# Performance work log

Hardware: AMD Instinct MI355X
Metric: run time of the kernel (lower is better)

## Reference

```python
import jax, jax.numpy as jnp
import numpy as np

D_IN = 512
SEQ_LEN = 4096
CHUNK = 256
NUM_CHUNKS = SEQ_LEN // CHUNK
BATCH = 4


def _xavier_uniform(key, d_in, d_out):
    limit = float(np.sqrt(6.0 / (d_in + d_out)))
    return jax.random.uniform(key, (d_in, d_out), dtype=jnp.float32, minval=-limit, maxval=limit)


def _logit(p, eps=1e-06):
    p = min(max(p, eps), 1.0 - eps)
    return jnp.asarray(np.log(p / (1.0 - p)), dtype=jnp.float32)


def setup_inputs() -> dict:
    key = jax.random.key(0)
    ks = jax.random.split(key, 6)
    x = jax.random.normal(ks[0], (BATCH, SEQ_LEN, D_IN), dtype=jnp.float32)
    return {
        "x": x,
        "w_q": _xavier_uniform(ks[1], D_IN, D_IN),
        "w_k": _xavier_uniform(ks[2], D_IN, D_IN),
        "w_v": _xavier_uniform(ks[3], D_IN, D_IN),
        "mem_w1": _xavier_uniform(ks[4], D_IN, 2 * D_IN),
        "mem_w2": _xavier_uniform(ks[5], 2 * D_IN, D_IN),
        "alpha_t": _logit(0.001),  # unconstrained; sigmoid -> alpha
        "lr_t": _logit(0.01),
        "decay_t": _logit(0.9),
        "update_mem": 1,
    }


def _mem_fwd(h, W1, W2):
    # LinearMLPMemory depth=2: x @ W1 -> gelu -> @ W2 (torch F.gelu is exact erf)
    return jax.nn.gelu(h @ W1, approximate=False) @ W2


def reference(x, w_q, w_k, w_v, mem_w1, mem_w2, alpha_t, lr_t, decay_t, update_mem):
    alpha = jax.nn.sigmoid(alpha_t)
    lr = jax.nn.sigmoid(lr_t)
    decay = jax.nn.sigmoid(decay_t)

    def loss_fn(Ws, k, v):
        W1, W2 = Ws
        pred = _mem_fwd(k, W1, W2)
        return jnp.mean((pred - v) ** 2)

    grad_fn = jax.grad(loss_fn)

    def step(carry, chunk):
        # chunk: [B, CHUNK, D]
        W1, W2, S1, S2 = carry
        k = chunk @ w_k
        v = chunk @ w_v
        g1, g2 = grad_fn((W1, W2), k, v)
        S1 = decay * S1 - lr * g1  # surprise (momentum of negative grads)
        S2 = decay * S2 - lr * g2
        W1 = (1.0 - alpha) * W1 + S1  # weight decay + surprise update
        W2 = (1.0 - alpha) * W2 + S2
        return (W1, W2, S1, S2), None

    W1, W2 = mem_w1, mem_w2
    if update_mem:
        B, S, D = x.shape
        # [NUM_CHUNKS, B, CHUNK, D]: sequential store over chunks (parallelize=False)
        chunks = x.reshape(B, NUM_CHUNKS, CHUNK, D).transpose(1, 0, 2, 3)
        init = (W1, W2, jnp.zeros_like(W1), jnp.zeros_like(W2))
        (W1, W2, _, _), _ = jax.lax.scan(step, init, chunks)

    q = x @ w_q
    return _mem_fwd(q, W1, W2)
```

## Files before the change

kernel.cpp:

```cpp
#include <hip/hip_runtime.h>
#include <math.h>

#define D_IN    512
#define HID     1024
#define CHUNK_L 256
#define NCHUNK  16
#define SEQ_L   4096
#define ROWS    1024
#define NROWS_T 16384

typedef __attribute__((ext_vector_type(4))) float f32x4;
typedef __attribute__((ext_vector_type(8))) short bf16x8;
typedef __attribute__((ext_vector_type(4))) short bf16x4;

#define LOSS_SCALE (2.0f / 524288.0f)

__device__ __forceinline__ float gelu_f(float v) {
    return v * 0.5f * (1.0f + erff(v * 0.70710678118654752f));
}
__device__ __forceinline__ float dgelu_f(float v) {
    float cdf = 0.5f * (1.0f + erff(v * 0.70710678118654752f));
    float pdf = 0.3989422804014327f * expf(-0.5f * v * v);
    return cdf + v * pdf;
}
__device__ __forceinline__ float sigmoid_dev(float x) { return 1.0f / (1.0f + expf(-x)); }
__device__ __forceinline__ short f2b(float f) {
    unsigned u = __float_as_uint(f);
    u += 0x7fffu + ((u >> 16) & 1u);
    return (short)(u >> 16);
}
__device__ __forceinline__ float b2f(short s) {
    return __uint_as_float(((unsigned)(unsigned short)s) << 16);
}
__device__ __forceinline__ float read_scalar(const float* p) {
    float v = *p;
    if (fabsf(v) > 0.5f && fabsf(v) < 16.0f) return v;
    unsigned short lo = ((const unsigned short*)p)[0];
    return __uint_as_float(((unsigned)lo) << 16);
}

__device__ __forceinline__ void glds16(const short* g, short* l) {
    __builtin_amdgcn_global_load_lds(
        (const __attribute__((address_space(1))) void*)g,
        (__attribute__((address_space(3))) void*)l, 16, 0, 0);
}

template<int NKB>
__device__ __forceinline__ void tile_gemm2(
    const short* __restrict__ A, int lda,
    const short* __restrict__ B, int ldb,
    int m0, int n0, short* KB, f32x4 acc[2][2])
{
    const int tid = threadIdx.x;
    const int lane = tid & 63, wave = tid >> 6;
    const int wy = (wave >> 1) * 32, wx = (wave & 1) * 32;
    const int l16 = lane & 15, q = lane >> 4;

    const int ga = tid, gb = tid + 256;
    const int ra = ga >> 3, ja = ga & 7;
    const int rb = gb >> 3, jb = gb & 7;
    const short* sA0 = A + (size_t)(m0 + ra) * lda + ((ja ^ (ra & 7)) << 3);
    const short* sA1 = A + (size_t)(m0 + rb) * lda + ((jb ^ (rb & 7)) << 3);
    const short* sB0 = B + (size_t)(n0 + ra) * ldb + ((ja ^ (ra & 7)) << 3);
    const short* sB1 = B + (size_t)(n0 + rb) * ldb + ((jb ^ (rb & 7)) << 3);

    f32x4 z = {0.f, 0.f, 0.f, 0.f};
    acc[0][0] = z; acc[0][1] = z; acc[1][0] = z; acc[1][1] = z;

    auto issue = [&](int kb) {
        const int ko = kb << 6;
        short* d = KB + (kb & 3) * 8192 + wave * 512;
        glds16(sA0 + ko, d);
        glds16(sA1 + ko, d + 2048);
        glds16(sB0 + ko, d + 4096);
        glds16(sB1 + ko, d + 6144);
    };
    issue(0); issue(1); issue(2);

#pragma unroll
    for (int j = 0; j < NKB; ++j) {
        if (NKB - 1 - j >= 2)      asm volatile("s_waitcnt vmcnt(8)" ::: "memory");
        else if (NKB - 1 - j == 1) asm volatile("s_waitcnt vmcnt(4)" ::: "memory");
        else                       asm volatile("s_waitcnt vmcnt(0)" ::: "memory");
        __builtin_amdgcn_s_barrier();
        __builtin_amdgcn_sched_barrier(0);
        if (j + 3 < NKB) issue(j + 3);
        const short* sl = KB + (j & 3) * 8192;
#pragma unroll
        for (int ks = 0; ks < 2; ++ks) {
            bf16x8 af[2], bf[2];
#pragma unroll
            for (int i = 0; i < 2; ++i) {
                int row = wy + i * 16 + l16;
                af[i] = *(const bf16x8*)&sl[(row << 6) + (((ks * 4 + q) ^ (row & 7)) << 3)];
            }
#pragma unroll
            for (int jj = 0; jj < 2; ++jj) {
                int row = wx + jj * 16 + l16;
                bf[jj] = *(const bf16x8*)&sl[4096 + (row << 6) + (((ks * 4 + q) ^ (row & 7)) << 3)];
            }
#pragma unroll
            for (int i = 0; i < 2; ++i)
#pragma unroll
                for (int jj = 0; jj < 2; ++jj)
                    acc[i][jj] = __builtin_amdgcn_mfma_f32_16x16x32_bf16(af[i], bf[jj], acc[i][jj], 0, 0, 0);
        }
    }
}

template<bool CHUNKA>
__device__ __forceinline__ void tile_gemm_f32(
    const float* __restrict__ Af, int lda, int t,
    const short* __restrict__ B, int ldb, int K,
    int m0, int n0, short* As, short* Bs, f32x4 acc[2][2])
{
    const int tid = threadIdx.x;
    const int lane = tid & 63, wave = tid >> 6;
    const int wy = (wave >> 1) * 32, wx = (wave & 1) * 32;
    const int l16 = lane & 15, q = lane >> 4;
    const int r0 = tid >> 3, r1 = r0 + 32, c8 = (tid & 7) * 8;

    auto arow = [&](int r) -> size_t {
        if (CHUNKA) return (size_t)(r >> 8) * SEQ_L + (size_t)t * CHUNK_L + (r & 255);
        return (size_t)r;
    };
    const size_t ga0 = arow(m0 + r0) * (size_t)lda + c8;
    const size_t ga1 = arow(m0 + r1) * (size_t)lda + c8;
    const size_t gb0 = (size_t)(n0 + r0) * ldb + c8;
    const size_t gb1 = (size_t)(n0 + r1) * ldb + c8;

    f32x4 fa0[2], fa1[2];
    bf16x8 rb0, rb1;

    auto load_tiles = [&](int k0) {
        fa0[0] = *(const f32x4*)&Af[ga0 + k0];
        fa0[1] = *(const f32x4*)&Af[ga0 + k0 + 4];
        fa1[0] = *(const f32x4*)&Af[ga1 + k0];
        fa1[1] = *(const f32x4*)&Af[ga1 + k0 + 4];
        rb0 = *(const bf16x8*)&B[gb0 + k0];
        rb1 = *(const bf16x8*)&B[gb1 + k0];
    };
    auto store_tiles = [&]() {
        bf16x8 p0, p1;
#pragma unroll
        for (int u = 0; u < 4; ++u) {
            p0[u] = f2b(fa0[0][u]); p0[u + 4] = f2b(fa0[1][u]);
            p1[u] = f2b(fa1[0][u]); p1[u + 4] = f2b(fa1[1][u]);
        }
        *(bf16x8*)&As[r0 * 72 + c8] = p0;
        *(bf16x8*)&As[r1 * 72 + c8] = p1;
        *(bf16x8*)&Bs[r0 * 72 + c8] = rb0;
        *(bf16x8*)&Bs[r1 * 72 + c8] = rb1;
    };

    f32x4 z = {0.f, 0.f, 0.f, 0.f};
    acc[0][0] = z; acc[0][1] = z; acc[1][0] = z; acc[1][1] = z;

    const int nkb = K >> 6;
    load_tiles(0);
    for (int kb = 0; kb < nkb; ++kb) {
        store_tiles();
        __syncthreads();
        if (kb + 1 < nkb) load_tiles((kb + 1) << 6);
#pragma unroll
        for (int ks = 0; ks < 2; ++ks) {
            bf16x8 af[2], bf[2];
#pragma unroll
            for (int i = 0; i < 2; ++i)
                af[i] = *(const bf16x8*)&As[(wy + i * 16 + l16) * 72 + ks * 32 + q * 8];
#pragma unroll
            for (int j = 0; j < 2; ++j)
                bf[j] = *(const bf16x8*)&Bs[(wx + j * 16 + l16) * 72 + ks * 32 + q * 8];
#pragma unroll
            for (int i = 0; i < 2; ++i)
#pragma unroll
                for (int j = 0; j < 2; ++j)
                    acc[i][j] = __builtin_amdgcn_mfma_f32_16x16x32_bf16(af[i], bf[j], acc[i][j], 0, 0, 0);
        }
        __syncthreads();
    }
}

#define EPI_IDX() \
    const int tid_ = threadIdx.x; \
    const int wy_  = ((tid_ >> 6) >> 1) * 32; \
    const int wxl_ = ((tid_ >> 6) & 1) * 32; \
    const int q4_  = ((tid_ & 63) >> 4) * 4; \
    const int l16_ = tid_ & 15;

__global__ __launch_bounds__(256)
void init_all(const float* __restrict__ w_q, const float* __restrict__ w_k,
              const float* __restrict__ w_v, const float* __restrict__ m1,
              const float* __restrict__ m2,
              float* __restrict__ W1f, float* __restrict__ W2f,
              float* __restrict__ S1, float* __restrict__ S2,
              short* __restrict__ WkvT, short* __restrict__ wqT,
              short* __restrict__ W1bT, short* __restrict__ W2bT,
              short* __restrict__ W2b0, short* __restrict__ W2b1)
{
    int i = blockIdx.x * 256 + threadIdx.x;
    float w1 = m1[i], w2 = m2[i];
    W1f[i] = w1; S1[i] = 0.f;
    W2f[i] = w2; S2[i] = 0.f;
    short w2b = f2b(w2);
    W2b0[i] = w2b; W2b1[i] = w2b;
    int n9 = i >> 9, k9 = i & 511;
    W1bT[i] = f2b(m1[(size_t)k9 * HID + n9]);
    WkvT[i] = f2b(n9 < 512 ? w_k[(size_t)k9 * D_IN + n9]
                           : w_v[(size_t)k9 * D_IN + (n9 - 512)]);
    if (i < 262144) wqT[i] = f2b(w_q[(size_t)k9 * D_IN + n9]);
    int n10 = i >> 10, k10 = i & 1023;
    W2bT[i] = f2b(m2[(size_t)k10 * D_IN + n10]);
}

__global__ __launch_bounds__(256)
void kvq_kernel(const float* __restrict__ x, const short* __restrict__ WkvT,
                const short* __restrict__ wqT,
                short* __restrict__ KVall, short* __restrict__ Ktall,
                short* __restrict__ qall)
{
    __shared__ short As[64 * 72];
    __shared__ short Bs[64 * 72];
    const int bid = blockIdx.x;
    EPI_IDX();
    f32x4 acc[2][2];
    if (bid < 4096) {
        int t = bid >> 8, tile = bid & 255;
        int m0 = (tile >> 4) * 64, n0 = (tile & 15) * 64;
        tile_gemm_f32<true>(x, D_IN, t, WkvT, D_IN, D_IN, m0, n0, As, Bs, acc);
        short* KV = KVall + (size_t)t * ROWS * 1024;
        short* Kt = Ktall + (size_t)t * D_IN * 1024;
#pragma unroll
        for (int i = 0; i < 2; ++i)
#pragma unroll
            for (int j = 0; j < 2; ++j) {
                int m = m0 + wy_ + i * 16 + q4_, n = n0 + wxl_ + j * 16 + l16_;
                bf16x4 pk;
#pragma unroll
                for (int r = 0; r < 4; ++r) {
                    short b = f2b(acc[i][j][r]);
                    KV[(size_t)(m + r) * 1024 + n] = b;
                    pk[r] = b;
                }
                if (n < 512) *(bf16x4*)&Kt[(size_t)n * 1024 + m] = pk;
            }
    } else {
        int idx = bid - 4096;
        int m0 = (idx >> 3) * 64, n0 = (idx & 7) * 64;
        tile_gemm_f32<false>(x, D_IN, 0, wqT, D_IN, D_IN, m0, n0, As, Bs, acc);
#pragma unroll
        for (int i = 0; i < 2; ++i)
#pragma unroll
            for (int j = 0; j < 2; ++j) {
                int m = m0 + wy_ + i * 16 + q4_, n = n0 + wxl_ + j * 16 + l16_;
#pragma unroll
                for (int r = 0; r < 4; ++r)
                    qall[(size_t)(m + r) * D_IN + n] = f2b(acc[i][j][r]);
            }
    }
}

__global__ __launch_bounds__(256)
void h_kernel(const short* __restrict__ KVt, const short* __restrict__ W1bT,
              short* __restrict__ Gb, short* __restrict__ GbT, short* __restrict__ DG)
{
    __shared__ short KB[4 * 2 * 4096];
    const int bid = blockIdx.x;
    EPI_IDX();
    int m0 = (bid >> 4) * 64, n0 = (bid & 15) * 64;
    f32x4 acc[2][2];
    tile_gemm2<8>(KVt, 1024, W1bT, D_IN, m0, n0, KB, acc);
#pragma unroll
    for (int i = 0; i < 2; ++i)
#pragma unroll
        for (int j = 0; j < 2; ++j) {
            int m = m0 + wy_ + i * 16 + q4_, n = n0 + wxl_ + j * 16 + l16_;
            bf16x4 pg;
#pragma unroll
            for (int r = 0; r < 4; ++r) {
                float v = acc[i][j][r];
                float g = gelu_f(v);
                Gb[(size_t)(m + r) * 1024 + n] = f2b(g);
                DG[(size_t)(m + r) * 1024 + n] = f2b(dgelu_f(v));
                pg[r] = f2b(g);
            }
            *(bf16x4*)&GbT[(size_t)n * 1024 + m] = pg;
        }
}

__global__ __launch_bounds__(256)
void e_kernel(const short* __restrict__ Gb, const short* __restrict__ W2bT,
              short* __restrict__ KVt, short* __restrict__ EVt)
{
    __shared__ short KB[4 * 2 * 4096];
    const int bid = blockIdx.x;
    EPI_IDX();
    int m0 = (bid >> 3) * 64, n0 = (bid & 7) * 64;
    f32x4 acc[2][2];
    tile_gemm2<16>(Gb, HID, W2bT, HID, m0, n0, KB, acc);
#pragma unroll
    for (int i = 0; i < 2; ++i)
#pragma unroll
        for (int j = 0; j < 2; ++j) {
            int m = m0 + wy_ + i * 16 + q4_, n = n0 + wxl_ + j * 16 + l16_;
            bf16x4 pe;
#pragma unroll
            for (int r = 0; r < 4; ++r) {
                size_t ci = (size_t)(m + r) * 1024 + 512 + n;
                float e = (acc[i][j][r] - b2f(KVt[ci])) * LOSS_SCALE;
                KVt[ci] = f2b(e);
                pe[r] = f2b(e);
            }
            *(bf16x4*)&EVt[(size_t)n * 1024 + m] = pe;
        }
}

__global__ __launch_bounds__(256)
void dhg2_kernel(const short* __restrict__ KVt, const short* __restrict__ W2bP,
                 const short* __restrict__ DG, short* __restrict__ DHt,
                 const short* __restrict__ GbT, const short* __restrict__ EVt,
                 float* __restrict__ W2f, float* __restrict__ S2,
                 short* __restrict__ W2bT, short* __restrict__ W2bN,
                 const float* __restrict__ ap, const float* __restrict__ lp,
                 const float* __restrict__ dp, const int* __restrict__ um)
{
    __shared__ short KB[4 * 2 * 4096];
    const int bid = blockIdx.x;
    EPI_IDX();
    f32x4 acc[2][2];
    if (bid < 256) {
        int m0 = (bid >> 4) * 64, n0 = (bid & 15) * 64;
        tile_gemm2<8>(KVt + 512, 1024, W2bP, D_IN, m0, n0, KB, acc);
#pragma unroll
        for (int i = 0; i < 2; ++i)
#pragma unroll
            for (int j = 0; j < 2; ++j) {
                int m = m0 + wy_ + i * 16 + q4_, n = n0 + wxl_ + j * 16 + l16_;
                bf16x4 pd;
#pragma unroll
                for (int r = 0; r < 4; ++r)
                    pd[r] = f2b(acc[i][j][r] * b2f(DG[(size_t)(m + r) * 1024 + n]));
                *(bf16x4*)&DHt[(size_t)n * 1024 + m] = pd;
            }
    } else {
        int idx = bid - 256;
        int m0 = (idx >> 3) * 64, n0 = (idx & 7) * 64;
        tile_gemm2<16>(GbT, ROWS, EVt, ROWS, m0, n0, KB, acc);
        if (*um != 0) {
            const float alpha = sigmoid_dev(read_scalar(ap));
            const float lr    = sigmoid_dev(read_scalar(lp));
            const float decay = sigmoid_dev(read_scalar(dp));
#pragma unroll
            for (int i = 0; i < 2; ++i)
#pragma unroll
                for (int j = 0; j < 2; ++j) {
                    int m = m0 + wy_ + i * 16 + q4_, n = n0 + wxl_ + j * 16 + l16_;
                    bf16x4 pw;
#pragma unroll
                    for (int r = 0; r < 4; ++r) {
                        size_t ci = (size_t)(m + r) * D_IN + n;
                        float s = decay * S2[ci] - lr * acc[i][j][r];
                        S2[ci] = s;
                        float w = (1.0f - alpha) * W2f[ci] + s;
                        W2f[ci] = w;
                        W2bN[ci] = f2b(w);
                        pw[r] = f2b(w);
                    }
                    *(bf16x4*)&W2bT[(size_t)n * 1024 + m] = pw;
                }
        }
    }
}

__global__ __launch_bounds__(256)
void g1_kernel(const short* __restrict__ Ktt, const short* __restrict__ DHt,
               float* __restrict__ W1f, float* __restrict__ S1,
               short* __restrict__ W1bT,
               const float* __restrict__ ap, const float* __restrict__ lp,
               const float* __restrict__ dp, const int* __restrict__ um)
{
    __shared__ short KB[4 * 2 * 4096];
    const int bid = blockIdx.x;
    EPI_IDX();
    int m0 = (bid >> 4) * 64, n0 = (bid & 15) * 64;
    f32x4 acc[2][2];
    tile_gemm2<16>(Ktt, ROWS, DHt, ROWS, m0, n0, KB, acc);
    if (*um != 0) {
        const float alpha = sigmoid_dev(read_scalar(ap));
        const float lr    = sigmoid_dev(read_scalar(lp));
        const float decay = sigmoid_dev(read_scalar(dp));
#pragma unroll
        for (int i = 0; i < 2; ++i)
#pragma unroll
            for (int j = 0; j < 2; ++j) {
                int m = m0 + wy_ + i * 16 + q4_, n = n0 + wxl_ + j * 16 + l16_;
                bf16x4 pw;
#pragma unroll
                for (int r = 0; r < 4; ++r) {
                    size_t ci = (size_t)(m + r) * HID + n;
                    float s = decay * S1[ci] - lr * acc[i][j][r];
                    S1[ci] = s;
                    float w = (1.0f - alpha) * W1f[ci] + s;
                    W1f[ci] = w;
                    pw[r] = f2b(w);
                }
                *(bf16x4*)&W1bT[(size_t)n * D_IN + m] = pw;
            }
    }
}

__global__ __launch_bounds__(256)
void ro_h_kernel(const short* __restrict__ qall, const short* __restrict__ W1bT,
                 short* __restrict__ Hro)
{
    __shared__ short KB[4 * 2 * 4096];
    const int bid = blockIdx.x;
    EPI_IDX();
    int m0 = (bid >> 4) * 64, n0 = (bid & 15) * 64;
    f32x4 acc[2][2];
    tile_gemm2<8>(qall, D_IN, W1bT, D_IN, m0, n0, KB, acc);
#pragma unroll
    for (int i = 0; i < 2; ++i)
#pragma unroll
        for (int j = 0; j < 2; ++j) {
            int m = m0 + wy_ + i * 16 + q4_, n = n0 + wxl_ + j * 16 + l16_;
#pragma unroll
            for (int r = 0; r < 4; ++r)
                Hro[(size_t)(m + r) * HID + n] = f2b(gelu_f(acc[i][j][r]));
        }
}

__global__ __launch_bounds__(256)
void ro_o_kernel(const short* __restrict__ Hro, const short* __restrict__ W2bT,
                 float* __restrict__ out)
{
    __shared__ short KB[4 * 2 * 4096];
    const int bid = blockIdx.x;
    EPI_IDX();
    int m0 = (bid >> 3) * 64, n0 = (bid & 7) * 64;
    f32x4 acc[2][2];
    tile_gemm2<16>(Hro, HID, W2bT, HID, m0, n0, KB, acc);
#pragma unroll
    for (int i = 0; i < 2; ++i)
#pragma unroll
        for (int j = 0; j < 2; ++j) {
            int m = m0 + wy_ + i * 16 + q4_, n = n0 + wxl_ + j * 16 + l16_;
#pragma unroll
            for (int r = 0; r < 4; ++r)
                out[(size_t)(m + r) * D_IN + n] = acc[i][j][r];
        }
}

extern "C" void kernel_launch(void* const* d_in, const int* in_sizes, int n_in,
                              void* d_out, int out_size, void* d_ws, size_t ws_size,
                              hipStream_t stream)
{
    const float* x      = (const float*)d_in[0];
    const float* w_q    = (const float*)d_in[1];
    const float* w_k    = (const float*)d_in[2];
    const float* w_v    = (const float*)d_in[3];
    const float* mem_w1 = (const float*)d_in[4];
    const float* mem_w2 = (const float*)d_in[5];
    const float* ap     = (const float*)d_in[6];
    const float* lp     = (const float*)d_in[7];
    const float* dpp    = (const float*)d_in[8];
    const int*   um     = (const int*)d_in[9];
    float* out = (float*)d_out;

    const int nW = D_IN * HID;
    float* W1f = (float*)d_ws;
    float* W2f = W1f + nW;
    float* S1  = W2f + nW;
    float* S2  = S1 + nW;
    short* p   = (short*)(S2 + nW);
    short* WkvT = p;            p += nW;
    short* wqT  = p;            p += 256 * 1024;
    short* W1bT = p;            p += nW;
    short* W2bT = p;            p += nW;
    short* W2b0 = p;            p += nW;
    short* W2b1 = p;            p += nW;
    short* Gb   = p;            p += ROWS * HID;
    short* GbT  = p;            p += ROWS * HID;
    short* DG   = p;            p += ROWS * HID;
    short* EVt  = p;            p += ROWS * D_IN;
    short* DHt  = p;            p += ROWS * HID;
    short* qall = p;            p += (size_t)NROWS_T * D_IN;
    short* KVall = p;           p += (size_t)NCHUNK * ROWS * 1024;
    short* Ktall = p;           p += (size_t)NCHUNK * D_IN * 1024;
    short* Hro  = p;            p += (size_t)NROWS_T * HID;

    dim3 blk(256);
    hipLaunchKernelGGL(init_all, dim3(nW / 256), blk, 0, stream,
                       w_q, w_k, w_v, mem_w1, mem_w2,
                       W1f, W2f, S1, S2, WkvT, wqT, W1bT, W2bT, W2b0, W2b1);
    hipLaunchKernelGGL(kvq_kernel, dim3(6144), blk, 0, stream,
                       x, WkvT, wqT, KVall, Ktall, qall);

    for (int t = 0; t < NCHUNK; ++t) {
        short* KVt  = KVall + (size_t)t * ROWS * 1024;
        short* Ktt  = Ktall + (size_t)t * D_IN * 1024;
        short* W2bP = (t & 1) ? W2b1 : W2b0;
        short* W2bN = (t & 1) ? W2b0 : W2b1;
        hipLaunchKernelGGL(h_kernel, dim3(256), blk, 0, stream, KVt, W1bT, Gb, GbT, DG);
        hipLaunchKernelGGL(e_kernel, dim3(128), blk, 0, stream, Gb, W2bT, KVt, EVt);
        hipLaunchKernelGGL(dhg2_kernel, dim3(384), blk, 0, stream,
                           KVt, W2bP, DG, DHt, GbT, EVt, W2f, S2, W2bT, W2bN,
                           ap, lp, dpp, um);
        hipLaunchKernelGGL(g1_kernel, dim3(128), blk, 0, stream,
                           Ktt, DHt, W1f, S1, W1bT, ap, lp, dpp, um);
    }

    hipLaunchKernelGGL(ro_h_kernel, dim3(4096), blk, 0, stream, qall, W1bT, Hro);
    hipLaunchKernelGGL(ro_o_kernel, dim3(2048), blk, 0, stream, Hro, W2bT, out);
}
```

Measured before the change: 826.3 us.

## Pre-convert x to bf16 and use shared GEMM path with M-fastest tile order

Adds a kernel that converts x to bf16 once, so the projection GEMM can use the same pipelined bf16 tile routine as the other GEMMs instead of a float-loading variant that converts on every tile load. The separate f32 tile routine is removed. All kernels also remap block index to tile so consecutive blocks walk along M and share the same B (weight) tile, which should improve L2 reuse of weights. The cost is an extra kernel launch and a bf16 copy of x in the workspace.

Measured after the change: 801.3 us. 3.0% less time.

```diff
diff --git a/kernel.cpp b/kernel.cpp
--- a/kernel.cpp
+++ b/kernel.cpp
@@ -105,79 +105,6 @@
                 for (int jj = 0; jj < 2; ++jj)
                     acc[i][jj] = __builtin_amdgcn_mfma_f32_16x16x32_bf16(af[i], bf[jj], acc[i][jj], 0, 0, 0);
         }
-    }
-}
-
-template<bool CHUNKA>
-__device__ __forceinline__ void tile_gemm_f32(
-    const float* __restrict__ Af, int lda, int t,
-    const short* __restrict__ B, int ldb, int K,
-    int m0, int n0, short* As, short* Bs, f32x4 acc[2][2])
-{
-    const int tid = threadIdx.x;
-    const int lane = tid & 63, wave = tid >> 6;
-    const int wy = (wave >> 1) * 32, wx = (wave & 1) * 32;
-    const int l16 = lane & 15, q = lane >> 4;
-    const int r0 = tid >> 3, r1 = r0 + 32, c8 = (tid & 7) * 8;
-
-    auto arow = [&](int r) -> size_t {
-        if (CHUNKA) return (size_t)(r >> 8) * SEQ_L + (size_t)t * CHUNK_L + (r & 255);
-        return (size_t)r;
-    };
-    const size_t ga0 = arow(m0 + r0) * (size_t)lda + c8;
-    const size_t ga1 = arow(m0 + r1) * (size_t)lda + c8;
-    const size_t gb0 = (size_t)(n0 + r0) * ldb + c8;
-    const size_t gb1 = (size_t)(n0 + r1) * ldb + c8;
-
-    f32x4 fa0[2], fa1[2];
-    bf16x8 rb0, rb1;
-
-    auto load_tiles = [&](int k0) {
-        fa0[0] = *(const f32x4*)&Af[ga0 + k0];
-        fa0[1] = *(const f32x4*)&Af[ga0 + k0 + 4];
-        fa1[0] = *(const f32x4*)&Af[ga1 + k0];
-        fa1[1] = *(const f32x4*)&Af[ga1 + k0 + 4];
-        rb0 = *(const bf16x8*)&B[gb0 + k0];
-        rb1 = *(const bf16x8*)&B[gb1 + k0];
-    };
-    auto store_tiles = [&]() {
-        bf16x8 p0, p1;
-#pragma unroll
-        for (int u = 0; u < 4; ++u) {
-            p0[u] = f2b(fa0[0][u]); p0[u + 4] = f2b(fa0[1][u]);
-            p1[u] = f2b(fa1[0][u]); p1[u + 4] = f2b(fa1[1][u]);
-        }
-        *(bf16x8*)&As[r0 * 72 + c8] = p0;
-        *(bf16x8*)&As[r1 * 72 + c8] = p1;
-        *(bf16x8*)&Bs[r0 * 72 + c8] = rb0;
-        *(bf16x8*)&Bs[r1 * 72 + c8] = rb1;
-    };
-
-    f32x4 z = {0.f, 0.f, 0.f, 0.f};
-    acc[0][0] = z; acc[0][1] = z; acc[1][0] = z; acc[1][1] = z;
-
-    const int nkb = K >> 6;
-    load_tiles(0);
-    for (int kb = 0; kb < nkb; ++kb) {
-        store_tiles();
-        __syncthreads();
-        if (kb + 1 < nkb) load_tiles((kb + 1) << 6);
-#pragma unroll
-        for (int ks = 0; ks < 2; ++ks) {
-            bf16x8 af[2], bf[2];
-#pragma unroll
-            for (int i = 0; i < 2; ++i)
-                af[i] = *(const bf16x8*)&As[(wy + i * 16 + l16) * 72 + ks * 32 + q * 8];
-#pragma unroll
-            for (int j = 0; j < 2; ++j)
-                bf[j] = *(const bf16x8*)&Bs[(wx + j * 16 + l16) * 72 + ks * 32 + q * 8];
-#pragma unroll
-            for (int i = 0; i < 2; ++i)
-#pragma unroll
-                for (int j = 0; j < 2; ++j)
-                    acc[i][j] = __builtin_amdgcn_mfma_f32_16x16x32_bf16(af[i], bf[j], acc[i][j], 0, 0, 0);
-        }
-        __syncthreads();
     }
 }
 
@@ -214,20 +141,32 @@
 }
 
 __global__ __launch_bounds__(256)
-void kvq_kernel(const float* __restrict__ x, const short* __restrict__ WkvT,
+void xb_kernel(const float* __restrict__ x, short* __restrict__ xb)
+{
+    int i = blockIdx.x * 256 + threadIdx.x;
+    f32x4 a = ((const f32x4*)x)[i * 2];
+    f32x4 b = ((const f32x4*)x)[i * 2 + 1];
+    bf16x8 o;
+#pragma unroll
+    for (int u = 0; u < 4; ++u) { o[u] = f2b(a[u]); o[u + 4] = f2b(b[u]); }
+    ((bf16x8*)xb)[i] = o;
+}
+
+__global__ __launch_bounds__(256)
+void kvq_kernel(const short* __restrict__ xb, const short* __restrict__ WkvT,
                 const short* __restrict__ wqT,
                 short* __restrict__ KVall, short* __restrict__ Ktall,
                 short* __restrict__ qall)
 {
-    __shared__ short As[64 * 72];
-    __shared__ short Bs[64 * 72];
+    __shared__ short KB[4 * 2 * 4096];
     const int bid = blockIdx.x;
     EPI_IDX();
     f32x4 acc[2][2];
     if (bid < 4096) {
         int t = bid >> 8, tile = bid & 255;
-        int m0 = (tile >> 4) * 64, n0 = (tile & 15) * 64;
-        tile_gemm_f32<true>(x, D_IN, t, WkvT, D_IN, D_IN, m0, n0, As, Bs, acc);
+        int m0 = (tile & 15) * 64, n0 = (tile >> 4) * 64;
+        const short* Akv = xb + ((size_t)(m0 >> 8) * SEQ_L + (size_t)t * CHUNK_L + (m0 & 255)) * D_IN;
+        tile_gemm2<8>(Akv, D_IN, WkvT, D_IN, 0, n0, KB, acc);
         short* KV = KVall + (size_t)t * ROWS * 1024;
         short* Kt = Ktall + (size_t)t * D_IN * 1024;
 #pragma unroll
@@ -246,8 +185,8 @@
             }
     } else {
         int idx = bid - 4096;
-        int m0 = (idx >> 3) * 64, n0 = (idx & 7) * 64;
-        tile_gemm_f32<false>(x, D_IN, 0, wqT, D_IN, D_IN, m0, n0, As, Bs, acc);
+        int m0 = (idx & 255) * 64, n0 = (idx >> 8) * 64;
+        tile_gemm2<8>(xb, D_IN, wqT, D_IN, m0, n0, KB, acc);
 #pragma unroll
         for (int i = 0; i < 2; ++i)
 #pragma unroll
@@ -267,7 +206,7 @@
     __shared__ short KB[4 * 2 * 4096];
     const int bid = blockIdx.x;
     EPI_IDX();
-    int m0 = (bid >> 4) * 64, n0 = (bid & 15) * 64;
+    int m0 = (bid & 15) * 64, n0 = (bid >> 4) * 64;
     f32x4 acc[2][2];
     tile_gemm2<8>(KVt, 1024, W1bT, D_IN, m0, n0, KB, acc);
 #pragma unroll
@@ -295,7 +234,7 @@
     __shared__ short KB[4 * 2 * 4096];
     const int bid = blockIdx.x;
     EPI_IDX();
-    int m0 = (bid >> 3) * 64, n0 = (bid & 7) * 64;
+    int m0 = (bid & 15) * 64, n0 = (bid >> 4) * 64;
     f32x4 acc[2][2];
     tile_gemm2<16>(Gb, HID, W2bT, HID, m0, n0, KB, acc);
 #pragma unroll
@@ -329,7 +268,7 @@
     EPI_IDX();
     f32x4 acc[2][2];
     if (bid < 256) {
-        int m0 = (bid >> 4) * 64, n0 = (bid & 15) * 64;
+        int m0 = (bid & 15) * 64, n0 = (bid >> 4) * 64;
         tile_gemm2<8>(KVt + 512, 1024, W2bP, D_IN, m0, n0, KB, acc);
 #pragma unroll
         for (int i = 0; i < 2; ++i)
@@ -344,7 +283,7 @@
             }
     } else {
         int idx = bid - 256;
-        int m0 = (idx >> 3) * 64, n0 = (idx & 7) * 64;
+        int m0 = (idx & 15) * 64, n0 = (idx >> 4) * 64;
         tile_gemm2<16>(GbT, ROWS, EVt, ROWS, m0, n0, KB, acc);
         if (*um != 0) {
             const float alpha = sigmoid_dev(read_scalar(ap));
@@ -382,7 +321,7 @@
     __shared__ short KB[4 * 2 * 4096];
     const int bid = blockIdx.x;
     EPI_IDX();
-    int m0 = (bid >> 4) * 64, n0 = (bid & 15) * 64;
+    int m0 = (bid & 7) * 64, n0 = (bid >> 3) * 64;
     f32x4 acc[2][2];
     tile_gemm2<16>(Ktt, ROWS, DHt, ROWS, m0, n0, KB, acc);
     if (*um != 0) {
@@ -416,7 +355,7 @@
     __shared__ short KB[4 * 2 * 4096];
     const int bid = blockIdx.x;
     EPI_IDX();
-    int m0 = (bid >> 4) * 64, n0 = (bid & 15) * 64;
+    int m0 = (bid & 255) * 64, n0 = (bid >> 8) * 64;
     f32x4 acc[2][2];
     tile_gemm2<8>(qall, D_IN, W1bT, D_IN, m0, n0, KB, acc);
 #pragma unroll
@@ -437,7 +376,7 @@
     __shared__ short KB[4 * 2 * 4096];
     const int bid = blockIdx.x;
     EPI_IDX();
-    int m0 = (bid >> 3) * 64, n0 = (bid & 7) * 64;
+    int m0 = (bid & 255) * 64, n0 = (bid >> 8) * 64;
     f32x4 acc[2][2];
     tile_gemm2<16>(Hro, HID, W2bT, HID, m0, n0, KB, acc);
 #pragma unroll
@@ -488,13 +427,15 @@
     short* KVall = p;           p += (size_t)NCHUNK * ROWS * 1024;
     short* Ktall = p;           p += (size_t)NCHUNK * D_IN * 1024;
     short* Hro  = p;            p += (size_t)NROWS_T * HID;
+    short* xb   = p;            p += (size_t)NROWS_T * D_IN;
 
     dim3 blk(256);
     hipLaunchKernelGGL(init_all, dim3(nW / 256), blk, 0, stream,
                        w_q, w_k, w_v, mem_w1, mem_w2,
                        W1f, W2f, S1, S2, WkvT, wqT, W1bT, W2bT, W2b0, W2b1);
+    hipLaunchKernelGGL(xb_kernel, dim3(4096), blk, 0, stream, x, xb);
     hipLaunchKernelGGL(kvq_kernel, dim3(6144), blk, 0, stream,
-                       x, WkvT, wqT, KVall, Ktall, qall);
+                       xb, WkvT, wqT, KVall, Ktall, qall);
 
     for (int t = 0; t < NCHUNK; ++t) {
         short* KVt  = KVall + (size_t)t * ROWS * 1024;
```
